# Performance work log

Hardware: AMD Instinct MI355X
Metric: run time of the kernel (lower is better)

## Reference

```python
import jax, jax.numpy as jnp
import numpy as np
from jax import lax

B, T, N, H, E = 128, 128, 49, 1024, 1024
EPS = 1e-6

def setup_inputs() -> dict:
    key = jax.random.key(0)
    ks = jax.random.split(key, 9)
    s = 0.02
    return {
        "X": jax.random.normal(ks[0], (B, T, E), jnp.float32),
        "G": jax.random.normal(ks[1], (2, B, H), jnp.float32),
        "L": jax.random.normal(ks[2], (B, N, H), jnp.float32),
        "W_ih0": jax.random.normal(ks[3], (3 * H, E), jnp.float32) * s,
        "W_hh0": jax.random.normal(ks[4], (3 * H, H), jnp.float32) * s,
        "W_ih1": jax.random.normal(ks[5], (3 * H, H), jnp.float32) * s,
        "W_hh1": jax.random.normal(ks[6], (3 * H, H), jnp.float32) * s,
        "W_lin": jax.random.normal(ks[7], (H, 2 * H), jnp.float32) * s,
        "a2": jnp.ones((H,), jnp.float32),
        "b2": jnp.zeros((H,), jnp.float32),
    }

def _gru_cell(x, h, W_ih, W_hh):
    # PyTorch GRUCell (bias=False): gates in order r, z, n
    gi = x @ W_ih.T  # [B, 3H]
    gh = h @ W_hh.T  # [B, 3H]
    i_r, i_z, i_n = jnp.split(gi, 3, axis=-1)
    h_r, h_z, h_n = jnp.split(gh, 3, axis=-1)
    r = jax.nn.sigmoid(i_r + h_r)
    z = jax.nn.sigmoid(i_z + h_z)
    n = jnp.tanh(i_n + r * h_n)
    return (1.0 - z) * n + z * h

def reference(X, G, L, W_ih0, W_hh0, W_ih1, W_hh1, W_lin, a2, b2):
    # NOTE: source attn() returns its input h (the bmm/softmax result is
    # discarded), so attention is dead code; dropout is eval-mode identity.
    def step(carry, xt):
        h0, h1_prev = carry            # each [B, H]
        h1 = _gru_cell(xt, h0, W_ih0, W_hh0)
        h2 = _gru_cell(h1, h1_prev, W_ih1, W_hh1)
        h_ = h2                        # drop (identity) + dead attn
        h0_new = jnp.tanh(jnp.concatenate([h0, h_], axis=1) @ W_lin.T)
        return (h0_new, h2), h0_new

    xs = jnp.swapaxes(X, 0, 1)         # [T, B, E]
    _, ys = lax.scan(step, (G[0], G[1]), xs)
    out = jnp.swapaxes(ys, 0, 1)       # [B, T, H]

    # LayerNorm with unbiased std and (std + eps) denominator (as in source)
    mean = out.mean(-1, keepdims=True)
    std = out.std(-1, ddof=1, keepdims=True)
    return a2 * (out - mean) / (std + EPS) + b2
```

## Files before the change

### kernel.cpp

```cpp
#include <hip/hip_runtime.h>
#include <hip/hip_bf16.h>

#define BB 128
#define TT 128
#define HH 1024
#define NWG 256
#define NT 512

typedef __bf16 bf16x8 __attribute__((ext_vector_type(8)));
typedef __bf16 bf16x4 __attribute__((ext_vector_type(4)));
typedef float  f32x4v __attribute__((ext_vector_type(4)));

#define MFMA16(a,b,c) __builtin_amdgcn_mfma_f32_16x16x32_bf16(a,b,c,0,0,0)

__device__ inline float fsig(float x) {
  x = fminf(fmaxf(x, -30.f), 30.f);
  return 1.f / (1.f + __expf(-x));
}
__device__ inline float ftanh(float x) {
  x = fminf(fmaxf(x, -15.f), 15.f);
  float e = __expf(2.f * x);
  return (e - 1.f) / (e + 1.f);
}
__device__ inline float bf2f(unsigned short u) {
  union { unsigned int i; float f; } c; c.i = (unsigned int)u << 16; return c.f;
}
__device__ inline void ucst16(__bf16* p, float v) {
  union { __bf16 b; unsigned short u; } c; c.b = (__bf16)v;
  __hip_atomic_store((unsigned short*)p, c.u, __ATOMIC_RELAXED, __HIP_MEMORY_SCOPE_AGENT);
}

#define SIGF(F) do { \
  __syncthreads(); \
  if (tid == 0) \
    __hip_atomic_store(&(F)[g * 16], t + 1, __ATOMIC_RELAXED, __HIP_MEMORY_SCOPE_AGENT); \
} while (0)

__device__ inline void wf1(const int* F, int tgt, int tid, int lane) {
  if (tid < 64) {
    while (__hip_atomic_load(&F[lane * 16], __ATOMIC_RELAXED, __HIP_MEMORY_SCOPE_AGENT) < tgt)
      __builtin_amdgcn_s_sleep(1);
    __builtin_amdgcn_fence(__ATOMIC_ACQUIRE, "agent");
  }
  __syncthreads();
  __builtin_amdgcn_sched_barrier(0);
}
__device__ inline void whalf(const int* F, int ch, int tgt, int tid, int lane) {
  if (tid < 64) {
    const int* P = F + (ch * 32 + (lane & 31)) * 16;
    while (__hip_atomic_load(P, __ATOMIC_RELAXED, __HIP_MEMORY_SCOPE_AGENT) < tgt)
      __builtin_amdgcn_s_sleep(1);
    __builtin_amdgcn_fence(__ATOMIC_ACQUIRE, "agent");
  }
  __syncthreads();
  __builtin_amdgcn_sched_barrier(0);
}

__device__ inline void stage_strip(char* dst, const float* src, int rstride, int tid) {
#pragma unroll
  for (int it = 0; it < 8; ++it) {
    int i = tid + it * NT;
    int rr = i >> 8;
    int c4 = i & 255;
    f32x4v v = *(const f32x4v*)(src + (size_t)rr * rstride + c4 * 4);
    bf16x4 o;
#pragma unroll
    for (int j = 0; j < 4; ++j) o[j] = (__bf16)v[j];
    *(bf16x4*)(dst + rr * 2048 + ((c4 * 8) ^ ((rr & 7) << 4))) = o;
  }
}

__device__ inline void stage_strip_b16(char* dst, const __bf16* src, int tid) {
#pragma unroll
  for (int it = 0; it < 8; ++it) {
    int i = tid + it * 256;
    int rr = i >> 7;
    int c8 = i & 127;
    bf16x8 v = *(const bf16x8*)(src + (size_t)rr * 1024 + c8 * 8);
    *(bf16x8*)(dst + rr * 2048 + ((c8 * 16) ^ ((rr & 7) << 4))) = v;
  }
}

template<int NS>
__device__ inline void gemm_half(const char* sm, const __bf16* __restrict__ A,
                                 int rowbase, int lane, int kb0, f32x4v (&acc)[NS]) {
  const int r = lane & 15, q = lane >> 4;
  const __bf16* Ap = A + (size_t)(rowbase + r) * 1024 + q * 8;
  bf16x8 a[16];
#pragma unroll
  for (int i = 0; i < 16; ++i) a[i] = *(const bf16x8*)(Ap + (kb0 + i) * 32);
  __builtin_amdgcn_sched_barrier(0);
  __builtin_amdgcn_s_setprio(1);
#pragma unroll
  for (int i = 0; i < 16; ++i) {
    const int kb = kb0 + i;
    const int byteo = (kb * 64 + q * 16) ^ ((r & 7) << 4);
#pragma unroll
    for (int s = 0; s < NS; ++s) {
      bf16x8 b = *(const bf16x8*)(sm + s * 32768 + r * 2048 + byteo);
      acc[s] = MFMA16(a[i], b, acc[s]);
    }
  }
  __builtin_amdgcn_s_setprio(0);
}

template<int NS>
__device__ inline void gemm_burst(const char* sm, const __bf16* __restrict__ A,
                                  int rowbase, int lane, f32x4v (&acc)[NS]) {
  const int r = lane & 15, q = lane >> 4;
  const __bf16* Ap = A + (size_t)(rowbase + r) * 1024 + q * 8;
  bf16x8 a[32];
#pragma unroll
  for (int kb = 0; kb < 32; ++kb) a[kb] = *(const bf16x8*)(Ap + kb * 32);
  __builtin_amdgcn_sched_barrier(0);
  __builtin_amdgcn_s_setprio(1);
#pragma unroll
  for (int kb = 0; kb < 32; ++kb) {
    const int byteo = (kb * 64 + q * 16) ^ ((r & 7) << 4);
#pragma unroll
    for (int s = 0; s < NS; ++s) {
      bf16x8 b = *(const bf16x8*)(sm + s * 32768 + r * 2048 + byteo);
      acc[s] = MFMA16(a[kb], b, acc[s]);
    }
  }
  __builtin_amdgcn_s_setprio(0);
}

__global__ void __launch_bounds__(NT, 2) gru_persist(
    const float* __restrict__ Whh0, const float* __restrict__ Wih1,
    const float* __restrict__ Whh1, const float* __restrict__ Wlin,
    const __bf16* __restrict__ gi0b, const float* __restrict__ G,
    __bf16* __restrict__ h0b, __bf16* __restrict__ h1b,
    __bf16* __restrict__ h2b, __bf16* __restrict__ gh1b,
    float* __restrict__ out, int* flags)
{
  __shared__ char sm[106496];
  float* h2s = (float*)(sm + 98304);
  const int tid = threadIdx.x, wg = blockIdx.x;
  const int wv = tid >> 6, lane = tid & 63;
  const int xcd = wg & 7;
  const int role = xcd >> 1;
  const int g = ((wg >> 3) << 1) | (xcd & 1);
  const int c0 = g * 16;
  const int r = lane & 15, q = lane >> 4;
  const bool gw = (wv < 4);

  if (role == 0) {
    stage_strip(sm,         Whh0 + (size_t)c0 * 1024,          1024, tid);
    stage_strip(sm + 32768, Whh0 + (size_t)(1024 + c0) * 1024, 1024, tid);
    stage_strip(sm + 65536, Whh0 + (size_t)(2048 + c0) * 1024, 1024, tid);
  } else if (role == 1) {
    stage_strip(sm,         Whh1 + (size_t)c0 * 1024,          1024, tid);
    stage_strip(sm + 32768, Whh1 + (size_t)(1024 + c0) * 1024, 1024, tid);
    stage_strip(sm + 65536, Whh1 + (size_t)(2048 + c0) * 1024, 1024, tid);
  } else if (role == 2) {
    stage_strip(sm,         Wih1 + (size_t)c0 * 1024,          1024, tid);
    stage_strip(sm + 32768, Wih1 + (size_t)(1024 + c0) * 1024, 1024, tid);
    stage_strip(sm + 65536, Wih1 + (size_t)(2048 + c0) * 1024, 1024, tid);
    for (int i = tid; i < 2048; i += NT) {
      int row = i >> 4, cc = i & 15;
      h2s[i] = G[131072 + row * 1024 + c0 + cc];
    }
  } else {
    stage_strip(sm,         Wlin + (size_t)c0 * 2048,        2048, tid);
    stage_strip(sm + 32768, Wlin + (size_t)c0 * 2048 + 1024, 2048, tid);
  }
  __syncthreads();

  int* F0h[2] = { flags + 0 * 1024, flags + 1 * 1024 };
  int* F1h[2] = { flags + 2 * 1024, flags + 3 * 1024 };
  int* F2h[2] = { flags + 4 * 1024, flags + 5 * 1024 };
  int* F3h[2] = { flags + 6 * 1024, flags + 7 * 1024 };

  if (role == 0) {
    for (int t = 0; t < TT; ++t) {
      __bf16* h1bP = h1b + (size_t)(t & 1) * 131072;
#pragma unroll
      for (int h = 0; h < 2; ++h) {
        const int rowbase = h * 64 + wv * 16;
        unsigned short pgr[4], pgz[4], pgn[4];
        if (gw) {
#pragma unroll
          for (int gg = 0; gg < 4; ++gg) {
            int row = rowbase + q * 4 + gg;
            const unsigned short* gp =
                (const unsigned short*)(gi0b + ((size_t)t * 128 + row) * 3072 + c0 + r);
            pgr[gg] = gp[0]; pgz[gg] = gp[1024]; pgn[gg] = gp[2048];
          }
        }
        f32x4v acc[3];
#pragma unroll
        for (int s = 0; s < 3; ++s) { f32x4v z = {0,0,0,0}; acc[s] = z; }
        whalf(F3h[h], 0, t, tid, lane);
        if (gw) gemm_half<3>(sm, h0b, rowbase, lane, 0, acc);
        whalf(F3h[h], 1, t, tid, lane);
        unsigned short ph[4];
        if (gw) {
#pragma unroll
          for (int gg = 0; gg < 4; ++gg) {
            int row = rowbase + q * 4 + gg;
            ph[gg] = *(const unsigned short*)(h0b + (size_t)row * 1024 + c0 + r);
          }
          gemm_half<3>(sm, h0b, rowbase, lane, 16, acc);
#pragma unroll
          for (int gg = 0; gg < 4; ++gg) {
            int row = rowbase + q * 4 + gg;
            float rv = fsig(bf2f(pgr[gg]) + acc[0][gg]);
            float zv = fsig(bf2f(pgz[gg]) + acc[1][gg]);
            float nv = ftanh(bf2f(pgn[gg]) + rv * acc[2][gg]);
            ucst16(h1bP + (size_t)row * 1024 + c0 + r, (1.f - zv) * nv + zv * bf2f(ph[gg]));
          }
        }
        SIGF(F0h[h]);
      }
    }
  } else if (role == 1) {
    for (int t = 0; t < TT; ++t) {
#pragma unroll
      for (int h = 0; h < 2; ++h) {
        wf1(F2h[h], t, tid, lane);
        if (gw) {
          const int rowbase = h * 64 + wv * 16;
          f32x4v acc[3];
#pragma unroll
          for (int s = 0; s < 3; ++s) { f32x4v z = {0,0,0,0}; acc[s] = z; }
          gemm_burst<3>(sm, h2b, rowbase, lane, acc);
#pragma unroll
          for (int gg = 0; gg < 4; ++gg) {
            size_t base = (size_t)(rowbase + q * 4 + gg) * 3072 + c0 + r;
            ucst16(gh1b + base,        acc[0][gg]);
            ucst16(gh1b + base + 1024, acc[1][gg]);
            ucst16(gh1b + base + 2048, acc[2][gg]);
          }
        }
        SIGF(F1h[h]);
      }
    }
  } else if (role == 2) {
    for (int t = 0; t < TT; ++t) {
      const __bf16* h1bP = h1b + (size_t)(t & 1) * 131072;
#pragma unroll
      for (int h = 0; h < 2; ++h) {
        const int rowbase = h * 64 + wv * 16;
        wf1(F1h[h], t + 1, tid, lane);
        unsigned short hg0[4], hg1[4], hg2[4];
        if (gw) {
#pragma unroll
          for (int gg = 0; gg < 4; ++gg) {
            int row = rowbase + q * 4 + gg;
            const unsigned short* hp = (const unsigned short*)(gh1b + (size_t)row * 3072 + c0 + r);
            hg0[gg] = hp[0]; hg1[gg] = hp[1024]; hg2[gg] = hp[2048];
          }
        }
        f32x4v acc[3];
#pragma unroll
        for (int s = 0; s < 3; ++s) { f32x4v z = {0,0,0,0}; acc[s] = z; }
        whalf(F0h[h], 0, t + 1, tid, lane);
        if (gw) gemm_half<3>(sm, h1bP, rowbase, lane, 0, acc);
        whalf(F0h[h], 1, t + 1, tid, lane);
        if (gw) {
          gemm_half<3>(sm, h1bP, rowbase, lane, 16, acc);
#pragma unroll
          for (int gg = 0; gg < 4; ++gg) {
            int row = rowbase + q * 4 + gg;
            float rv = fsig(acc[0][gg] + bf2f(hg0[gg]));
            float zv = fsig(acc[1][gg] + bf2f(hg1[gg]));
            float nv = ftanh(acc[2][gg] + rv * bf2f(hg2[gg]));
            float hp = h2s[row * 16 + r];
            float h2 = (1.f - zv) * nv + zv * hp;
            h2s[row * 16 + r] = h2;
            ucst16(h2b + (size_t)row * 1024 + c0 + r, h2);
          }
        }
        SIGF(F2h[h]);
      }
    }
  } else {
    for (int t = 0; t < TT; ++t) {
#pragma unroll
      for (int h = 0; h < 2; ++h) {
        const int rowbase = h * 64 + wv * 16;
        wf1(F3h[h], t, tid, lane);
        f32x4v accL[1];
        { f32x4v z = {0,0,0,0}; accL[0] = z; }
        if (gw) gemm_burst<1>(sm, h0b, rowbase, lane, accL);
        f32x4v accR[1];
        { f32x4v z = {0,0,0,0}; accR[0] = z; }
        whalf(F2h[h], 0, t + 1, tid, lane);
        if (gw) gemm_half<1>(sm + 32768, h2b, rowbase, lane, 0, accR);
        whalf(F2h[h], 1, t + 1, tid, lane);
        if (gw) {
          gemm_half<1>(sm + 32768, h2b, rowbase, lane, 16, accR);
#pragma unroll
          for (int gg = 0; gg < 4; ++gg) {
            int row = rowbase + q * 4 + gg;
            float v = ftanh(accL[0][gg] + accR[0][gg]);
            ucst16(h0b + (size_t)row * 1024 + c0 + r, v);
            out[((size_t)row * 128 + t) * 1024 + c0 + r] = v;
          }
        }
        SIGF(F3h[h]);
      }
    }
  }
}

__global__ void __launch_bounds__(256) gi0_kernel(const float* __restrict__ X,
                                                  const __bf16* __restrict__ Wih0b,
                                                  __bf16* __restrict__ gi0b) {
  __shared__ char sm[131072];
  const int tid = threadIdx.x, wv = tid >> 6, lane = tid & 63;
  const int bi = blockIdx.x;
  const int n = bi % 48, mg = bi / 48;
#pragma unroll
  for (int s = 0; s < 4; ++s)
    stage_strip_b16(sm + s * 32768, Wih0b + (size_t)(n * 64 + s * 16) * 1024, tid);
  __syncthreads();
  const int r = lane & 15, q = lane >> 4;
  for (int mi = mg * 4; mi < mg * 4 + 4; ++mi) {
    f32x4v acc[4][2];
#pragma unroll
    for (int s = 0; s < 4; ++s) { f32x4v z = {0,0,0,0}; acc[s][0] = z; acc[s][1] = z; }
    const float* Ap = X + ((size_t)mi * 128 + wv * 32 + r) * 1024 + q * 8;
#pragma unroll 4
    for (int kb = 0; kb < 32; ++kb) {
      f32x4v x0a = *(const f32x4v*)(Ap + kb * 32);
      f32x4v x0b = *(const f32x4v*)(Ap + kb * 32 + 4);
      f32x4v x1a = *(const f32x4v*)(Ap + 16384 + kb * 32);
      f32x4v x1b = *(const f32x4v*)(Ap + 16384 + kb * 32 + 4);
      bf16x8 a0, a1;
#pragma unroll
      for (int j = 0; j < 4; ++j) {
        a0[j] = (__bf16)x0a[j]; a0[4 + j] = (__bf16)x0b[j];
        a1[j] = (__bf16)x1a[j]; a1[4 + j] = (__bf16)x1b[j];
      }
      const int byteo = (kb * 64 + q * 16) ^ ((r & 7) << 4);
#pragma unroll
      for (int s = 0; s < 4; ++s) {
        bf16x8 b = *(const bf16x8*)(sm + s * 32768 + r * 2048 + byteo);
        acc[s][0] = MFMA16(a0, b, acc[s][0]);
        acc[s][1] = MFMA16(a1, b, acc[s][1]);
      }
    }
#pragma unroll
    for (int s = 0; s < 4; ++s)
#pragma unroll
      for (int mf = 0; mf < 2; ++mf)
#pragma unroll
        for (int gg = 0; gg < 4; ++gg) {
          int trow = wv * 32 + mf * 16 + q * 4 + gg;
          gi0b[((size_t)trow * 128 + mi) * 3072 + n * 64 + s * 16 + r] = (__bf16)acc[s][mf][gg];
        }
  }
}

__global__ void __launch_bounds__(256) prep3(const float* __restrict__ Wih0f,
                                             const float* __restrict__ G,
                                             __bf16* Wih0b,
                                             __bf16* h0b, __bf16* h2b, int* flags) {
  long c = (long)blockIdx.x * 256 + threadIdx.x;
  if (c < 786432) {
    f32x4v v = *(const f32x4v*)(Wih0f + c * 4);
    bf16x4 o;
#pragma unroll
    for (int j = 0; j < 4; ++j) o[j] = (__bf16)v[j];
    *(bf16x4*)(Wih0b + c * 4) = o;
  } else if (c < 786432 + 131072) {
    long i = c - 786432;
    h0b[i] = (__bf16)G[i];
  } else if (c < 786432 + 262144) {
    long i = c - 786432 - 131072;
    h2b[i] = (__bf16)G[131072 + i];
  } else if (c < 786432 + 262144 + 8192) {
    flags[c - 786432 - 262144] = 0;
  }
}

__global__ void __launch_bounds__(256) ln_kernel(float* __restrict__ out,
                                                 const float* __restrict__ a2,
                                                 const float* __restrict__ b2) {
  int wv = threadIdx.x >> 6, lane = threadIdx.x & 63;
  size_t row = (size_t)blockIdx.x * 4 + wv;
  float* p = out + row * 1024;
  f32x4v v[4];
  float s = 0.f, ss = 0.f;
#pragma unroll
  for (int i = 0; i < 4; ++i) {
    v[i] = *(const f32x4v*)(p + (i * 64 + lane) * 4);
#pragma unroll
    for (int j = 0; j < 4; ++j) { s += v[i][j]; ss += v[i][j] * v[i][j]; }
  }
#pragma unroll
  for (int o = 32; o > 0; o >>= 1) { s += __shfl_xor(s, o); ss += __shfl_xor(ss, o); }
  float mean = s * (1.f / 1024.f);
  float var = (ss - 1024.f * mean * mean) * (1.f / 1023.f);
  var = fmaxf(var, 0.f);
  float inv = 1.f / (sqrtf(var) + 1e-6f);
#pragma unroll
  for (int i = 0; i < 4; ++i) {
    int c0 = (i * 64 + lane) * 4;
    f32x4v gA = *(const f32x4v*)(a2 + c0);
    f32x4v bo = *(const f32x4v*)(b2 + c0);
    f32x4v o;
#pragma unroll
    for (int j = 0; j < 4; ++j) o[j] = gA[j] * (v[i][j] - mean) * inv + bo[j];
    *(f32x4v*)(p + c0) = o;
  }
}

extern "C" void kernel_launch(void* const* d_in, const int* in_sizes, int n_in,
                              void* d_out, int out_size, void* d_ws, size_t ws_size,
                              hipStream_t stream) {
  const float* X    = (const float*)d_in[0];
  const float* G    = (const float*)d_in[1];
  const float* Wih0 = (const float*)d_in[3];
  const float* Whh0 = (const float*)d_in[4];
  const float* Wih1 = (const float*)d_in[5];
  const float* Whh1 = (const float*)d_in[6];
  const float* Wlin = (const float*)d_in[7];
  const float* a2   = (const float*)d_in[8];
  const float* b2   = (const float*)d_in[9];
  float* out = (float*)d_out;

  char* ws = (char*)d_ws;
  size_t off = 0;
  auto take = [&](size_t n) { char* p = ws + off; off += (n + 255) & ~(size_t)255; return p; };
  __bf16* Wih0b = (__bf16*)take((size_t)3072 * 1024 * 2);
  __bf16* gi0b  = (__bf16*)take((size_t)16384 * 3072 * 2);
  __bf16* gh1b  = (__bf16*)take((size_t)128 * 3072 * 2);
  __bf16* h0b   = (__bf16*)take((size_t)BB * HH * 2);
  __bf16* h1b   = (__bf16*)take((size_t)BB * HH * 2 * 2);
  __bf16* h2b   = (__bf16*)take((size_t)BB * HH * 2);
  int*    flags = (int*)take(8192 * 4);
  if (off > ws_size) return;

  prep3<<<4128, 256, 0, stream>>>(Wih0, G, Wih0b, h0b, h2b, flags);
  gi0_kernel<<<1536, 256, 0, stream>>>(X, Wih0b, gi0b);
  gru_persist<<<NWG, NT, 0, stream>>>(Whh0, Wih1, Whh1, Wlin, gi0b, G,
                                      h0b, h1b, h2b, gh1b, out, flags);
  ln_kernel<<<4096, 256, 0, stream>>>(out, a2, b2);
}
```

Baseline: 4.075 ms.

## Use atomic counters for inter-workgroup sync and vectorize transposed MFMA outputs

Per-workgroup flag arrays are replaced with shared atomic counters per role, batch half and column half. Waiters now poll one or two counters instead of 32–64 separate flag slots. The MFMA operands are swapped so each lane holds four consecutive columns of one row. This allows 64-bit bf16 stores and 128-bit float stores instead of scalar 16-bit stores, and the h2 shared-memory buffer is padded to stride 17 to avoid bank conflicts. The trade-off is contention on the fetch_add counters, since 32 workgroups increment each one.

```diff
diff --git a/kernel.cpp b/kernel.cpp
--- a/kernel.cpp
+++ b/kernel.cpp
@@ -22,32 +22,33 @@
   float e = __expf(2.f * x);
   return (e - 1.f) / (e + 1.f);
 }
-__device__ inline float bf2f(unsigned short u) {
-  union { unsigned int i; float f; } c; c.i = (unsigned int)u << 16; return c.f;
-}
-__device__ inline void ucst16(__bf16* p, float v) {
-  union { __bf16 b; unsigned short u; } c; c.b = (__bf16)v;
-  __hip_atomic_store((unsigned short*)p, c.u, __ATOMIC_RELAXED, __HIP_MEMORY_SCOPE_AGENT);
-}
-
-#define SIGF(F) do { \
+__device__ inline void ucst64(__bf16* p, const f32x4v v) {
+  union { unsigned long long u; __bf16 b[4]; } c;
+#pragma unroll
+  for (int j = 0; j < 4; ++j) c.b[j] = (__bf16)v[j];
+  __hip_atomic_store((unsigned long long*)p, c.u, __ATOMIC_RELAXED, __HIP_MEMORY_SCOPE_AGENT);
+}
+
+#define CPTR(role,bh,ch) (flags + (((role)*2+(bh))*2+(ch))*16)
+
+#define SIGC(role,bh) do { \
   __syncthreads(); \
   if (tid == 0) \
-    __hip_atomic_store(&(F)[g * 16], t + 1, __ATOMIC_RELAXED, __HIP_MEMORY_SCOPE_AGENT); \
+    __hip_atomic_fetch_add(CPTR(role,bh,chg), 1, __ATOMIC_RELAXED, __HIP_MEMORY_SCOPE_AGENT); \
 } while (0)
 
-__device__ inline void wf1(const int* F, int tgt, int tid, int lane) {
+__device__ inline void cwait1(const int* C, int tgt, int tid) {
   if (tid < 64) {
-    while (__hip_atomic_load(&F[lane * 16], __ATOMIC_RELAXED, __HIP_MEMORY_SCOPE_AGENT) < tgt)
+    while (__hip_atomic_load(C, __ATOMIC_RELAXED, __HIP_MEMORY_SCOPE_AGENT) < tgt)
       __builtin_amdgcn_s_sleep(1);
     __builtin_amdgcn_fence(__ATOMIC_ACQUIRE, "agent");
   }
   __syncthreads();
   __builtin_amdgcn_sched_barrier(0);
 }
-__device__ inline void whalf(const int* F, int ch, int tgt, int tid, int lane) {
+__device__ inline void cwait2(const int* C0, const int* C1, int tgt, int tid, int lane) {
   if (tid < 64) {
-    const int* P = F + (ch * 32 + (lane & 31)) * 16;
+    const int* P = (lane < 32) ? C0 : C1;
     while (__hip_atomic_load(P, __ATOMIC_RELAXED, __HIP_MEMORY_SCOPE_AGENT) < tgt)
       __builtin_amdgcn_s_sleep(1);
     __builtin_amdgcn_fence(__ATOMIC_ACQUIRE, "agent");
@@ -98,7 +99,7 @@
 #pragma unroll
     for (int s = 0; s < NS; ++s) {
       bf16x8 b = *(const bf16x8*)(sm + s * 32768 + r * 2048 + byteo);
-      acc[s] = MFMA16(a[i], b, acc[s]);
+      acc[s] = MFMA16(b, a[i], acc[s]);
     }
   }
   __builtin_amdgcn_s_setprio(0);
@@ -120,7 +121,7 @@
 #pragma unroll
     for (int s = 0; s < NS; ++s) {
       bf16x8 b = *(const bf16x8*)(sm + s * 32768 + r * 2048 + byteo);
-      acc[s] = MFMA16(a[kb], b, acc[s]);
+      acc[s] = MFMA16(b, a[kb], acc[s]);
     }
   }
   __builtin_amdgcn_s_setprio(0);
@@ -134,7 +135,7 @@
     __bf16* __restrict__ h2b, __bf16* __restrict__ gh1b,
     float* __restrict__ out, int* flags)
 {
-  __shared__ char sm[106496];
+  __shared__ char sm[107008];
   float* h2s = (float*)(sm + 98304);
   const int tid = threadIdx.x, wg = blockIdx.x;
   const int wv = tid >> 6, lane = tid & 63;
@@ -142,6 +143,7 @@
   const int role = xcd >> 1;
   const int g = ((wg >> 3) << 1) | (xcd & 1);
   const int c0 = g * 16;
+  const int chg = (g >= 32);
   const int r = lane & 15, q = lane >> 4;
   const bool gw = (wv < 4);
 
@@ -159,7 +161,7 @@
     stage_strip(sm + 65536, Wih1 + (size_t)(2048 + c0) * 1024, 1024, tid);
     for (int i = tid; i < 2048; i += NT) {
       int row = i >> 4, cc = i & 15;
-      h2s[i] = G[131072 + row * 1024 + c0 + cc];
+      h2s[row * 17 + cc] = G[131072 + row * 1024 + c0 + cc];
     }
   } else {
     stage_strip(sm,         Wlin + (size_t)c0 * 2048,        2048, tid);
@@ -167,73 +169,60 @@
   }
   __syncthreads();
 
-  int* F0h[2] = { flags + 0 * 1024, flags + 1 * 1024 };
-  int* F1h[2] = { flags + 2 * 1024, flags + 3 * 1024 };
-  int* F2h[2] = { flags + 4 * 1024, flags + 5 * 1024 };
-  int* F3h[2] = { flags + 6 * 1024, flags + 7 * 1024 };
-
   if (role == 0) {
     for (int t = 0; t < TT; ++t) {
       __bf16* h1bP = h1b + (size_t)(t & 1) * 131072;
 #pragma unroll
       for (int h = 0; h < 2; ++h) {
         const int rowbase = h * 64 + wv * 16;
-        unsigned short pgr[4], pgz[4], pgn[4];
-        if (gw) {
+        const int row = rowbase + r;
+        bf16x4 vgr, vgz, vgn;
+        if (gw) {
+          const __bf16* gp = gi0b + ((size_t)t * 128 + row) * 3072 + c0 + q * 4;
+          vgr = *(const bf16x4*)(gp);
+          vgz = *(const bf16x4*)(gp + 1024);
+          vgn = *(const bf16x4*)(gp + 2048);
+        }
+        f32x4v acc[3];
+#pragma unroll
+        for (int s = 0; s < 3; ++s) { f32x4v z = {0,0,0,0}; acc[s] = z; }
+        cwait1(CPTR(3,h,0), 32 * t, tid);
+        if (gw) gemm_half<3>(sm, h0b, rowbase, lane, 0, acc);
+        cwait1(CPTR(3,h,1), 32 * t, tid);
+        if (gw) {
+          bf16x4 vph = *(const bf16x4*)(h0b + (size_t)row * 1024 + c0 + q * 4);
+          gemm_half<3>(sm, h0b, rowbase, lane, 16, acc);
+          f32x4v o;
 #pragma unroll
           for (int gg = 0; gg < 4; ++gg) {
-            int row = rowbase + q * 4 + gg;
-            const unsigned short* gp =
-                (const unsigned short*)(gi0b + ((size_t)t * 128 + row) * 3072 + c0 + r);
-            pgr[gg] = gp[0]; pgz[gg] = gp[1024]; pgn[gg] = gp[2048];
+            float rv = fsig((float)vgr[gg] + acc[0][gg]);
+            float zv = fsig((float)vgz[gg] + acc[1][gg]);
+            float nv = ftanh((float)vgn[gg] + rv * acc[2][gg]);
+            o[gg] = (1.f - zv) * nv + zv * (float)vph[gg];
           }
-        }
-        f32x4v acc[3];
-#pragma unroll
-        for (int s = 0; s < 3; ++s) { f32x4v z = {0,0,0,0}; acc[s] = z; }
-        whalf(F3h[h], 0, t, tid, lane);
-        if (gw) gemm_half<3>(sm, h0b, rowbase, lane, 0, acc);
-        whalf(F3h[h], 1, t, tid, lane);
-        unsigned short ph[4];
-        if (gw) {
-#pragma unroll
-          for (int gg = 0; gg < 4; ++gg) {
-            int row = rowbase + q * 4 + gg;
-            ph[gg] = *(const unsigned short*)(h0b + (size_t)row * 1024 + c0 + r);
-          }
-          gemm_half<3>(sm, h0b, rowbase, lane, 16, acc);
-#pragma unroll
-          for (int gg = 0; gg < 4; ++gg) {
-            int row = rowbase + q * 4 + gg;
-            float rv = fsig(bf2f(pgr[gg]) + acc[0][gg]);
-            float zv = fsig(bf2f(pgz[gg]) + acc[1][gg]);
-            float nv = ftanh(bf2f(pgn[gg]) + rv * acc[2][gg]);
-            ucst16(h1bP + (size_t)row * 1024 + c0 + r, (1.f - zv) * nv + zv * bf2f(ph[gg]));
-          }
-        }
-        SIGF(F0h[h]);
+          ucst64(h1bP + (size_t)row * 1024 + c0 + q * 4, o);
+        }
+        SIGC(0, h);
       }
     }
   } else if (role == 1) {
     for (int t = 0; t < TT; ++t) {
 #pragma unroll
       for (int h = 0; h < 2; ++h) {
-        wf1(F2h[h], t, tid, lane);
+        cwait2(CPTR(2,h,0), CPTR(2,h,1), 32 * t, tid, lane);
         if (gw) {
           const int rowbase = h * 64 + wv * 16;
+          const int row = rowbase + r;
           f32x4v acc[3];
 #pragma unroll
           for (int s = 0; s < 3; ++s) { f32x4v z = {0,0,0,0}; acc[s] = z; }
           gemm_burst<3>(sm, h2b, rowbase, lane, acc);
-#pragma unroll
-          for (int gg = 0; gg < 4; ++gg) {
-            size_t base = (size_t)(rowbase + q * 4 + gg) * 3072 + c0 + r;
-            ucst16(gh1b + base,        acc[0][gg]);
-            ucst16(gh1b + base + 1024, acc[1][gg]);
-            ucst16(gh1b + base + 2048, acc[2][gg]);
-          }
-        }
-        SIGF(F1h[h]);
+          size_t base = (size_t)row * 3072 + c0 + q * 4;
+          ucst64(gh1b + base,        acc[0]);
+          ucst64(gh1b + base + 1024, acc[1]);
+          ucst64(gh1b + base + 2048, acc[2]);
+        }
+        SIGC(1, h);
       }
     }
   } else if (role == 2) {
@@ -242,37 +231,37 @@
 #pragma unroll
       for (int h = 0; h < 2; ++h) {
         const int rowbase = h * 64 + wv * 16;
-        wf1(F1h[h], t + 1, tid, lane);
-        unsigned short hg0[4], hg1[4], hg2[4];
-        if (gw) {
+        const int row = rowbase + r;
+        cwait2(CPTR(1,h,0), CPTR(1,h,1), 32 * (t + 1), tid, lane);
+        bf16x4 vh0, vh1, vh2;
+        if (gw) {
+          const __bf16* hp = gh1b + (size_t)row * 3072 + c0 + q * 4;
+          vh0 = *(const bf16x4*)(hp);
+          vh1 = *(const bf16x4*)(hp + 1024);
+          vh2 = *(const bf16x4*)(hp + 2048);
+        }
+        f32x4v acc[3];
+#pragma unroll
+        for (int s = 0; s < 3; ++s) { f32x4v z = {0,0,0,0}; acc[s] = z; }
+        cwait1(CPTR(0,h,0), 32 * (t + 1), tid);
+        if (gw) gemm_half<3>(sm, h1bP, rowbase, lane, 0, acc);
+        cwait1(CPTR(0,h,1), 32 * (t + 1), tid);
+        if (gw) {
+          gemm_half<3>(sm, h1bP, rowbase, lane, 16, acc);
+          f32x4v o;
 #pragma unroll
           for (int gg = 0; gg < 4; ++gg) {
-            int row = rowbase + q * 4 + gg;
-            const unsigned short* hp = (const unsigned short*)(gh1b + (size_t)row * 3072 + c0 + r);
-            hg0[gg] = hp[0]; hg1[gg] = hp[1024]; hg2[gg] = hp[2048];
+            float rv = fsig(acc[0][gg] + (float)vh0[gg]);
+            float zv = fsig(acc[1][gg] + (float)vh1[gg]);
+            float nv = ftanh(acc[2][gg] + rv * (float)vh2[gg]);
+            float hp2 = h2s[row * 17 + q * 4 + gg];
+            float h2 = (1.f - zv) * nv + zv * hp2;
+            h2s[row * 17 + q * 4 + gg] = h2;
+            o[gg] = h2;
           }
-        }
-        f32x4v acc[3];
-#pragma unroll
-        for (int s = 0; s < 3; ++s) { f32x4v z = {0,0,0,0}; acc[s] = z; }
-        whalf(F0h[h], 0, t + 1, tid, lane);
-        if (gw) gemm_half<3>(sm, h1bP, rowbase, lane, 0, acc);
-        whalf(F0h[h], 1, t + 1, tid, lane);
-        if (gw) {
-          gemm_half<3>(sm, h1bP, rowbase, lane, 16, acc);
-#pragma unroll
-          for (int gg = 0; gg < 4; ++gg) {
-            int row = rowbase + q * 4 + gg;
-            float rv = fsig(acc[0][gg] + bf2f(hg0[gg]));
-            float zv = fsig(acc[1][gg] + bf2f(hg1[gg]));
-            float nv = ftanh(acc[2][gg] + rv * bf2f(hg2[gg]));
-            float hp = h2s[row * 16 + r];
-            float h2 = (1.f - zv) * nv + zv * hp;
-            h2s[row * 16 + r] = h2;
-            ucst16(h2b + (size_t)row * 1024 + c0 + r, h2);
-          }
-        }
-        SIGF(F2h[h]);
+          ucst64(h2b + (size_t)row * 1024 + c0 + q * 4, o);
+        }
+        SIGC(2, h);
       }
     }
   } else {
@@ -280,26 +269,26 @@
 #pragma unroll
       for (int h = 0; h < 2; ++h) {
         const int rowbase = h * 64 + wv * 16;
-        wf1(F3h[h], t, tid, lane);
+        const int row = rowbase + r;
+        cwait2(CPTR(3,h,0), CPTR(3,h,1), 32 * t, tid, lane);
         f32x4v accL[1];
         { f32x4v z = {0,0,0,0}; accL[0] = z; }
         if (gw) gemm_burst<1>(sm, h0b, rowbase, lane, accL);
         f32x4v accR[1];
         { f32x4v z = {0,0,0,0}; accR[0] = z; }
-        whalf(F2h[h], 0, t + 1, tid, lane);
+        cwait1(CPTR(2,h,0), 32 * (t + 1), tid);
         if (gw) gemm_half<1>(sm + 32768, h2b, rowbase, lane, 0, accR);
-        whalf(F2h[h], 1, t + 1, tid, lane);
+        cwait1(CPTR(2,h,1), 32 * (t + 1), tid);
         if (gw) {
           gemm_half<1>(sm + 32768, h2b, rowbase, lane, 16, accR);
-#pragma unroll
-          for (int gg = 0; gg < 4; ++gg) {
-            int row = rowbase + q * 4 + gg;
-            float v = ftanh(accL[0][gg] + accR[0][gg]);
-            ucst16(h0b + (size_t)row * 1024 + c0 + r, v);
-            out[((size_t)row * 128 + t) * 1024 + c0 + r] = v;
-          }
-        }
-        SIGF(F3h[h]);
+          f32x4v o;
+#pragma unroll
+          for (int gg = 0; gg < 4; ++gg)
+            o[gg] = ftanh(accL[0][gg] + accR[0][gg]);
+          ucst64(h0b + (size_t)row * 1024 + c0 + q * 4, o);
+          *(f32x4v*)(out + ((size_t)row * 128 + t) * 1024 + c0 + q * 4) = o;
+        }
+        SIGC(3, h);
       }
     }
   }
```

New measurement: 4.119 ms. About the same (+1.1%).
